# Kernel tuning notes

Hardware: AMD Instinct MI355X
Metric: run time of the kernel (lower is better)

Reference implementation:

```python
import jax, jax.numpy as jnp
import numpy as np

N = 50000   # nodes
E = 800000  # directed edges
D = 128     # input_channels


def _kaiming(key, shape):
    fan_in = shape[0]
    return jax.random.normal(key, shape, jnp.float32) * np.float32(np.sqrt(2.0 / fan_in))


def setup_inputs():
    key = jax.random.key(0)
    ks = jax.random.split(key, 8)
    x = jax.random.normal(ks[0], (N, D), jnp.float32)
    edge_index = jax.random.randint(ks[1], (2, E), 0, N, dtype=jnp.int32)
    return {
        "x": x,
        "edge_index": edge_index,
        "W_in": _kaiming(ks[2], (D, D)),      "b_in": jnp.zeros((D,), jnp.float32),
        "W1": _kaiming(ks[3], (D, 2 * D)),    "b1": jnp.zeros((2 * D,), jnp.float32),
        "W2": _kaiming(ks[4], (2 * D, D)),    "b2": jnp.zeros((D,), jnp.float32),
        "W3": _kaiming(ks[5], (D, D // 2)),   "b3": jnp.zeros((D // 2,), jnp.float32),
        "W_out": _kaiming(ks[6], (D // 2, 1)), "b_out": jnp.zeros((1,), jnp.float32),
    }


def _gcn_conv(x, src, dst, W, b, n):
    """PyG GCNConv: add self-loops, symmetric D^-1/2 (A+I) D^-1/2 normalization."""
    h = x @ W  # [n, out]
    loop = jnp.arange(n, dtype=src.dtype)
    s = jnp.concatenate([src, loop])  # message sources (x_j)
    d = jnp.concatenate([dst, loop])  # aggregation targets (x_i)
    deg = jax.ops.segment_sum(jnp.ones_like(d, jnp.float32), d, num_segments=n)
    dis = jnp.where(deg > 0, jax.lax.rsqrt(jnp.maximum(deg, 1.0)), 0.0)
    norm = dis[s] * dis[d]  # [E+n]
    msg = h[s] * norm[:, None]  # gather + scale
    out = jax.ops.segment_sum(msg, d, num_segments=n)  # scatter-add
    return out + b


def reference(x, edge_index, W_in, b_in, W1, b1, W2, b2, W3, b3, W_out, b_out):
    src, dst = edge_index[0], edge_index[1]
    n = x.shape[0]
    lrelu = lambda t: jax.nn.leaky_relu(t, 0.01)
    # dropout in eval mode (identity)
    h = lrelu(x @ W_in + b_in)
    h = lrelu(_gcn_conv(h, src, dst, W1, b1, n))
    h = lrelu(_gcn_conv(h, src, dst, W2, b2, n))
    h = lrelu(_gcn_conv(h, src, dst, W3, b3, n))
    return h @ W_out + b_out  # [n, 1]
```

## Files before the change

### kernel.cpp

```cpp
#include <hip/hip_runtime.h>


#define LRELU(v) ((v) > 0.f ? (v) : 0.01f * (v))

typedef __attribute__((ext_vector_type(8))) _Float16 half8;
typedef __attribute__((ext_vector_type(8))) float float8;
typedef __attribute__((ext_vector_type(4))) float floatx4;


__global__ __launch_bounds__(256) void k_count(const int* __restrict__ dst,
                                               int* __restrict__ cnt, int E) {
  int e = blockIdx.x * 256 + threadIdx.x;
  if (e < E) atomicAdd(&cnt[dst[e]], 1);
}

__global__ __launch_bounds__(256) void k_scan1(const int* __restrict__ cnt,
                                               int* __restrict__ offs,
                                               int* __restrict__ bsum,
                                               float* __restrict__ dis, int N) {
  __shared__ int s[256];
  const int t = threadIdx.x;
  const int i = blockIdx.x * 256 + t;
  const int v = (i < N) ? cnt[i] : 0;
  s[t] = v;
  __syncthreads();
#pragma unroll
  for (int off = 1; off < 256; off <<= 1) {
    int u = (t >= off) ? s[t - off] : 0;
    __syncthreads();
    s[t] += u;
    __syncthreads();
  }
  if (i < N) {
    offs[i] = s[t] - v;
    dis[i] = rsqrtf((float)v + 1.0f);
  }
  if (t == 255) bsum[blockIdx.x] = s[255];
}

__global__ __launch_bounds__(256) void k_scan2(int* __restrict__ bsum, int nb) {
  __shared__ int s[256];
  const int t = threadIdx.x;
  const int v = (t < nb) ? bsum[t] : 0;
  s[t] = v;
  __syncthreads();
#pragma unroll
  for (int off = 1; off < 256; off <<= 1) {
    int u = (t >= off) ? s[t - off] : 0;
    __syncthreads();
    s[t] += u;
    __syncthreads();
  }
  if (t < nb) bsum[t] = s[t] - v;
}

__global__ __launch_bounds__(256) void k_scan3(int* __restrict__ offs,
                                               const int* __restrict__ bsum,
                                               int N, int E) {
  const int i = blockIdx.x * 256 + threadIdx.x;
  if (i < N) offs[i] += bsum[blockIdx.x];
  if (i == 0) offs[N] = E;
}

__global__ __launch_bounds__(256) void k_fill(const int* __restrict__ src,
                                              const int* __restrict__ dst,
                                              const int* __restrict__ offs,
                                              int* __restrict__ cur,
                                              int* __restrict__ esrc,
                                              int E, int PR) {
  const int e = blockIdx.x * 256 + threadIdx.x;
  int d = -1, s = 0, pd = 0;
  if (e < E) {
    d = dst[e];
    s = src[e];
    pd = d / PR;
  }
#pragma unroll
  for (int p = 0; p < 8; ++p) {
    if (e < E && pd == p) {
      const int pos = offs[d] + atomicAdd(&cur[d], 1);
      esrc[pos] = s;
    }
    __syncthreads();
  }
}

__global__ __launch_bounds__(256) void k_wtall(const float* __restrict__ W_in,
                                               const float* __restrict__ W1,
                                               const float* __restrict__ W2,
                                               const float* __restrict__ W3,
                                               _Float16* __restrict__ wt_in,
                                               _Float16* __restrict__ wt1,
                                               _Float16* __restrict__ wt2,
                                               _Float16* __restrict__ wt3) {
  const int idx = blockIdx.x * 256 + threadIdx.x;
  const int m = blockIdx.y;
  if (m == 0) {
    if (idx < 128 * 128) {
      const int k = idx >> 7, f = idx & 127;
      wt_in[f * 128 + k] = (_Float16)W_in[idx];
    }
  } else if (m == 1) {
    if (idx < 128 * 256) {
      const int k = idx >> 8, f = idx & 255;
      wt1[f * 128 + k] = (_Float16)W1[idx];
    }
  } else if (m == 2) {
    if (idx < 256 * 128) {
      const int k = idx >> 7, f = idx & 127;
      wt2[f * 256 + k] = (_Float16)W2[idx];
    }
  } else {
    if (idx < 128 * 64) {
      const int k = idx >> 6, f = idx & 63;
      wt3[f * 128 + k] = (_Float16)W3[idx];
    }
  }
}

template <int K, int F, int EPI, typename IT>
__global__ __launch_bounds__(256) void k_gemm(const IT* __restrict__ X,
                                              const _Float16* __restrict__ Wt,
                                              const float* __restrict__ b,
                                              const float* __restrict__ dis,
                                              _Float16* __restrict__ out, int M) {
  constexpr int TM = 64;
  constexpr int PAD = 8;
  constexpr int LK = K + PAD;
  constexpr int CW = F / 4;
  constexpr int NT = CW / 16;
  constexpr int NK = K / 32;
  __shared__ _Float16 xs[TM * LK];

  const int m0 = blockIdx.x * TM;
  const int tid = threadIdx.x;
  const int w = tid >> 6;
  const int lane = tid & 63;
  const int m = lane & 15;
  const int q = lane >> 4;

  half8 breg[NT][NK];
#pragma unroll
  for (int t = 0; t < NT; ++t)
#pragma unroll
    for (int kc = 0; kc < NK; ++kc)
      breg[t][kc] =
          *(const half8*)&Wt[(long)(w * CW + t * 16 + m) * K + kc * 32 + q * 8];

  constexpr int CPR = K / 8;
  for (int idx = tid; idx < TM * CPR; idx += 256) {
    const int row = idx / CPR;
    const int kk = idx % CPR;
    const int g = m0 + row;
    half8 h = (half8)(_Float16)0.f;
    if (g < M) {
      if constexpr (sizeof(IT) == 4) {
        const float4* p = (const float4*)&X[(long)g * K + kk * 8];
        float4 a = p[0], c = p[1];
        h[0] = (_Float16)a.x; h[1] = (_Float16)a.y;
        h[2] = (_Float16)a.z; h[3] = (_Float16)a.w;
        h[4] = (_Float16)c.x; h[5] = (_Float16)c.y;
        h[6] = (_Float16)c.z; h[7] = (_Float16)c.w;
      } else {
        h = *(const half8*)&X[(long)g * K + kk * 8];
      }
    }
    *(half8*)&xs[row * LK + kk * 8] = h;
  }
  __syncthreads();

  floatx4 acc[4][NT];
#pragma unroll
  for (int rt = 0; rt < 4; ++rt)
#pragma unroll
    for (int t = 0; t < NT; ++t) acc[rt][t] = (floatx4){0.f, 0.f, 0.f, 0.f};

#pragma unroll
  for (int kc = 0; kc < NK; ++kc) {
    half8 af[4];
#pragma unroll
    for (int rt = 0; rt < 4; ++rt)
      af[rt] = *(const half8*)&xs[(rt * 16 + m) * LK + kc * 32 + q * 8];
#pragma unroll
    for (int rt = 0; rt < 4; ++rt)
#pragma unroll
      for (int t = 0; t < NT; ++t)
        acc[rt][t] = __builtin_amdgcn_mfma_f32_16x16x32_f16(af[rt], breg[t][kc],
                                                            acc[rt][t], 0, 0, 0);
  }

#pragma unroll
  for (int rt = 0; rt < 4; ++rt) {
#pragma unroll
    for (int r = 0; r < 4; ++r) {
      const int row = m0 + rt * 16 + q * 4 + r;
      if (row < M) {
        float dv = 1.f;
        if constexpr (EPI != 1) dv = dis[row];
#pragma unroll
        for (int t = 0; t < NT; ++t) {
          const int col = w * CW + t * 16 + m;
          float v = acc[rt][t][r];
          if constexpr (EPI == 0) { v += b[col]; v = LRELU(v); v *= dv; }
          if constexpr (EPI == 1) { v += b[col]; v = LRELU(v); }
          if constexpr (EPI == 2) { v *= dv; }
          out[(long)row * F + col] = (_Float16)v;
        }
      }
    }
  }
}

template <int F, int MODE>
__global__ __launch_bounds__(256) void k_agg(const _Float16* __restrict__ G,
                                             const int* __restrict__ esrc,
                                             const int* __restrict__ offs,
                                             const float* __restrict__ dis,
                                             const float* __restrict__ b,
                                             const float* __restrict__ Wout,
                                             const float* __restrict__ bout,
                                             void* __restrict__ out, int N) {
  constexpr int CH = F / 8;
  const int w = threadIdx.x >> 6;
  const int i = blockIdx.x * 4 + w;
  if (i >= N) return;
  const int lane = threadIdx.x & 63;
  const int c = lane & (CH - 1);
  const int j = lane / CH;
  constexpr int JS = 64 / CH;

  float8 acc = {0.f, 0.f, 0.f, 0.f, 0.f, 0.f, 0.f, 0.f};
  if (j == 0)
    acc = __builtin_convertvector(*(const half8*)&G[(long)i * F + c * 8], float8);
  const int e0 = offs[i], e1 = offs[i + 1];
  for (int e = e0 + j; e < e1; e += JS) {
    const int s = esrc[e];
    acc += __builtin_convertvector(*(const half8*)&G[(long)s * F + c * 8], float8);
  }
#pragma unroll
  for (int off = CH; off < 64; off <<= 1)
#pragma unroll
    for (int k = 0; k < 8; ++k) acc[k] += __shfl_xor(acc[k], off);

  const float dv = dis[i];
  if constexpr (MODE == 2) {
    float p = 0.f;
#pragma unroll
    for (int k = 0; k < 8; ++k) {
      const int col = c * 8 + k;
      float v = acc[k] * dv + b[col];
      v = LRELU(v);
      p += v * Wout[col];
    }
#pragma unroll
    for (int off = 1; off < CH; off <<= 1) p += __shfl_xor(p, off);
    if (lane == 0) ((float*)out)[i] = p + bout[0];
  } else {
    if (j == 0) {
      half8 hv;
#pragma unroll
      for (int k = 0; k < 8; ++k) {
        float v = acc[k] * dv;
        if constexpr (MODE == 1) { v += b[c * 8 + k]; v = LRELU(v); }
        hv[k] = (_Float16)v;
      }
      *(half8*)&((_Float16*)out)[(long)i * F + c * 8] = hv;
    }
  }
}


extern "C" void kernel_launch(void* const* d_in, const int* in_sizes, int n_in,
                              void* d_out, int out_size, void* d_ws, size_t ws_size,
                              hipStream_t stream) {
  const float* x     = (const float*)d_in[0];
  const int* eidx    = (const int*)d_in[1];
  const float* W_in  = (const float*)d_in[2];
  const float* b_in  = (const float*)d_in[3];
  const float* W1    = (const float*)d_in[4];
  const float* b1    = (const float*)d_in[5];
  const float* W2    = (const float*)d_in[6];
  const float* b2    = (const float*)d_in[7];
  const float* W3    = (const float*)d_in[8];
  const float* b3    = (const float*)d_in[9];
  const float* W_out = (const float*)d_in[10];
  const float* b_out = (const float*)d_in[11];
  float* out = (float*)d_out;

  const int N = in_sizes[0] / 128;
  const int E = in_sizes[1] / 2;
  const int* src = eidx;
  const int* dst = eidx + E;
  const int nb = (N + 255) / 256;
  const int PR = (N + 7) / 8;

  size_t off = 0;
  char* base = (char*)d_ws;
  auto alloc = [&](size_t bytes) -> void* {
    void* p = base + off;
    off = (off + bytes + 255) & ~(size_t)255;
    return p;
  };
  int* cnt        = (int*)alloc((size_t)2 * N * sizeof(int));
  int* cur        = cnt + N;
  int* offs       = (int*)alloc((size_t)(N + 4) * sizeof(int));
  int* bsum       = (int*)alloc(256 * sizeof(int));
  int* esrc       = (int*)alloc((size_t)E * sizeof(int));
  float* dis      = (float*)alloc((size_t)N * sizeof(float));
  _Float16* wt_in = (_Float16*)alloc((size_t)128 * 128 * 2);
  _Float16* wt1   = (_Float16*)alloc((size_t)256 * 128 * 2);
  _Float16* wt2   = (_Float16*)alloc((size_t)128 * 256 * 2);
  _Float16* wt3   = (_Float16*)alloc((size_t)64 * 128 * 2);
  _Float16* buf1  = (_Float16*)alloc((size_t)N * 128 * 2);
  _Float16* buf2  = (_Float16*)alloc((size_t)N * 128 * 2);
  _Float16* buf3  = (_Float16*)alloc((size_t)N * 256 * 2);

  hipMemsetAsync(cnt, 0, (size_t)2 * N * sizeof(int), stream);

  const int gE = (E + 255) / 256;
  const int gRows = (N + 63) / 64;
  const int gAgg = (N + 3) / 4;

  k_wtall<<<dim3(128, 4), 256, 0, stream>>>(W_in, W1, W2, W3,
                                            wt_in, wt1, wt2, wt3);
  k_count<<<gE, 256, 0, stream>>>(dst, cnt, E);
  k_scan1<<<nb, 256, 0, stream>>>(cnt, offs, bsum, dis, N);
  k_scan2<<<1, 256, 0, stream>>>(bsum, nb);
  k_scan3<<<nb, 256, 0, stream>>>(offs, bsum, N, E);
  k_fill<<<gE, 256, 0, stream>>>(src, dst, offs, cur, esrc, E, PR);

  k_gemm<128, 128, 0, float><<<gRows, 256, 0, stream>>>(x, wt_in, b_in, dis,
                                                        buf1, N);
  k_agg<128, 0><<<gAgg, 256, 0, stream>>>(buf1, esrc, offs, dis, nullptr,
                                          nullptr, nullptr, buf2, N);
  k_gemm<128, 256, 1, _Float16><<<gRows, 256, 0, stream>>>(buf2, wt1, b1,
                                                           nullptr, buf3, N);
  k_gemm<256, 128, 2, _Float16><<<gRows, 256, 0, stream>>>(buf3, wt2, nullptr,
                                                           dis, buf1, N);
  k_agg<128, 1><<<gAgg, 256, 0, stream>>>(buf1, esrc, offs, dis, b2,
                                          nullptr, nullptr, buf2, N);
  k_gemm<128, 64, 2, _Float16><<<gRows, 256, 0, stream>>>(buf2, wt3, nullptr,
                                                          dis, buf3, N);
  k_agg<64, 2><<<gAgg, 256, 0, stream>>>(buf3, esrc, offs, dis, b3,
                                         W_out, b_out, out, N);
}
```

Baseline: 339.2 us.

## Split aggregation columns across grid and pack two nodes per wave; merge scan kernels

The aggregation kernel now has each wave handle two nodes, with 8 lanes covering 64 columns and 4 edge streams per node. For F=128 the column range is split across a second grid dimension, so each block reads only half of each gathered row and the per-row working set shrinks. The reduction drops from a full-wave shuffle to two shuffle steps. The scan2 and scan3 kernels are merged so that each block reduces the preceding block sums itself, saving one launch at the cost of redundant per-block reductions. Edge indices are read twice in the F=128 layers because of the column split.

Result: no change. 334.0 us (-1.5%).

```diff
diff --git a/kernel.cpp b/kernel.cpp
--- a/kernel.cpp
+++ b/kernel.cpp
@@ -38,27 +38,22 @@
   if (t == 255) bsum[blockIdx.x] = s[255];
 }
 
-__global__ __launch_bounds__(256) void k_scan2(int* __restrict__ bsum, int nb) {
+__global__ __launch_bounds__(256) void k_scan3(int* __restrict__ offs,
+                                               const int* __restrict__ bsum,
+                                               int N, int E, int nb) {
   __shared__ int s[256];
   const int t = threadIdx.x;
-  const int v = (t < nb) ? bsum[t] : 0;
-  s[t] = v;
+  const int b = blockIdx.x;
+  s[t] = (t < b && t < nb) ? bsum[t] : 0;
   __syncthreads();
 #pragma unroll
-  for (int off = 1; off < 256; off <<= 1) {
-    int u = (t >= off) ? s[t - off] : 0;
+  for (int off = 128; off > 0; off >>= 1) {
+    if (t < off) s[t] += s[t + off];
     __syncthreads();
-    s[t] += u;
-    __syncthreads();
-  }
-  if (t < nb) bsum[t] = s[t] - v;
-}
-
-__global__ __launch_bounds__(256) void k_scan3(int* __restrict__ offs,
-                                               const int* __restrict__ bsum,
-                                               int N, int E) {
-  const int i = blockIdx.x * 256 + threadIdx.x;
-  if (i < N) offs[i] += bsum[blockIdx.x];
+  }
+  const int add = s[0];
+  const int i = b * 256 + t;
+  if (i < N) offs[i] += add;
   if (i == 0) offs[N] = E;
 }
 
@@ -220,27 +215,32 @@
                                              const float* __restrict__ Wout,
                                              const float* __restrict__ bout,
                                              void* __restrict__ out, int N) {
-  constexpr int CH = F / 8;
   const int w = threadIdx.x >> 6;
-  const int i = blockIdx.x * 4 + w;
-  if (i >= N) return;
   const int lane = threadIdx.x & 63;
-  const int c = lane & (CH - 1);
-  const int j = lane / CH;
-  constexpr int JS = 64 / CH;
-
+  const int c = lane & 7;
+  const int j = lane >> 3;
+  const int n = j >> 2;
+  const int jj = j & 3;
+  const int i0 = blockIdx.x * 8 + w * 2;
+  int i = i0 + n;
+  const bool valid = (i < N);
+  if (!valid) i = N - 1;
+  const int col0 = (F == 128) ? (blockIdx.y << 6) : 0;
+
+  const _Float16* gbase = G + col0 + c * 8;
   float8 acc = {0.f, 0.f, 0.f, 0.f, 0.f, 0.f, 0.f, 0.f};
-  if (j == 0)
-    acc = __builtin_convertvector(*(const half8*)&G[(long)i * F + c * 8], float8);
+  if (jj == 0)
+    acc = __builtin_convertvector(*(const half8*)(gbase + (long)i * F), float8);
   const int e0 = offs[i], e1 = offs[i + 1];
-  for (int e = e0 + j; e < e1; e += JS) {
-    const int s = esrc[e];
-    acc += __builtin_convertvector(*(const half8*)&G[(long)s * F + c * 8], float8);
-  }
-#pragma unroll
-  for (int off = CH; off < 64; off <<= 1)
-#pragma unroll
-    for (int k = 0; k < 8; ++k) acc[k] += __shfl_xor(acc[k], off);
+  for (int e = e0 + jj; e < e1; e += 4) {
+    acc += __builtin_convertvector(
+        *(const half8*)(gbase + (long)esrc[e] * F), float8);
+  }
+#pragma unroll
+  for (int k = 0; k < 8; ++k) {
+    acc[k] += __shfl_xor(acc[k], 8);
+    acc[k] += __shfl_xor(acc[k], 16);
+  }
 
   const float dv = dis[i];
   if constexpr (MODE == 2) {
@@ -252,19 +252,20 @@
       v = LRELU(v);
       p += v * Wout[col];
     }
-#pragma unroll
-    for (int off = 1; off < CH; off <<= 1) p += __shfl_xor(p, off);
-    if (lane == 0) ((float*)out)[i] = p + bout[0];
+    p += __shfl_xor(p, 1);
+    p += __shfl_xor(p, 2);
+    p += __shfl_xor(p, 4);
+    if (valid && jj == 0 && c == 0) ((float*)out)[i] = p + bout[0];
   } else {
-    if (j == 0) {
+    if (valid && jj == 0) {
       half8 hv;
 #pragma unroll
       for (int k = 0; k < 8; ++k) {
         float v = acc[k] * dv;
-        if constexpr (MODE == 1) { v += b[c * 8 + k]; v = LRELU(v); }
+        if constexpr (MODE == 1) { v += b[col0 + c * 8 + k]; v = LRELU(v); }
         hv[k] = (_Float16)v;
       }
-      *(half8*)&((_Float16*)out)[(long)i * F + c * 8] = hv;
+      *(half8*)&((_Float16*)out)[(long)i * F + col0 + c * 8] = hv;
     }
   }
 }
@@ -319,28 +320,28 @@
 
   const int gE = (E + 255) / 256;
   const int gRows = (N + 63) / 64;
-  const int gAgg = (N + 3) / 4;
+  const int gAggP = (N + 7) / 8;
 
   k_wtall<<<dim3(128, 4), 256, 0, stream>>>(W_in, W1, W2, W3,
                                             wt_in, wt1, wt2, wt3);
   k_count<<<gE, 256, 0, stream>>>(dst, cnt, E);
   k_scan1<<<nb, 256, 0, stream>>>(cnt, offs, bsum, dis, N);
-  k_scan2<<<1, 256, 0, stream>>>(bsum, nb);
-  k_scan3<<<nb, 256, 0, stream>>>(offs, bsum, N, E);
+  k_scan3<<<nb, 256, 0, stream>>>(offs, bsum, N, E, nb);
   k_fill<<<gE, 256, 0, stream>>>(src, dst, offs, cur, esrc, E, PR);
 
   k_gemm<128, 128, 0, float><<<gRows, 256, 0, stream>>>(x, wt_in, b_in, dis,
                                                         buf1, N);
-  k_agg<128, 0><<<gAgg, 256, 0, stream>>>(buf1, esrc, offs, dis, nullptr,
-                                          nullptr, nullptr, buf2, N);
+  k_agg<128, 0><<<dim3(gAggP, 2), 256, 0, stream>>>(buf1, esrc, offs, dis,
+                                                    nullptr, nullptr, nullptr,
+                                                    buf2, N);
   k_gemm<128, 256, 1, _Float16><<<gRows, 256, 0, stream>>>(buf2, wt1, b1,
                                                            nullptr, buf3, N);
   k_gemm<256, 128, 2, _Float16><<<gRows, 256, 0, stream>>>(buf3, wt2, nullptr,
                                                            dis, buf1, N);
-  k_agg<128, 1><<<gAgg, 256, 0, stream>>>(buf1, esrc, offs, dis, b2,
-                                          nullptr, nullptr, buf2, N);
+  k_agg<128, 1><<<dim3(gAggP, 2), 256, 0, stream>>>(buf1, esrc, offs, dis, b2,
+                                                    nullptr, nullptr, buf2, N);
   k_gemm<128, 64, 2, _Float16><<<gRows, 256, 0, stream>>>(buf2, wt3, nullptr,
                                                           dis, buf3, N);
-  k_agg<64, 2><<<gAgg, 256, 0, stream>>>(buf3, esrc, offs, dis, b3,
-                                         W_out, b_out, out, N);
-}
+  k_agg<64, 2><<<gAggP, 256, 0, stream>>>(buf3, esrc, offs, dis, b3,
+                                          W_out, b_out, out, N);
+}
```
